# Performance work log

Measured on AMD Instinct MI355X. Metric: run time of the kernel, lower is better.

Reference implementation:

```python
import jax, jax.numpy as jnp
import numpy as np

SOS = 1
H = 1024   # hidden_size
V = 32000  # vocab_size
B = 64     # batch
S = 50     # encoder (source) length
T = 25     # decode steps (target length)


def setup_inputs() -> dict:
    key = jax.random.key(0)
    ks = jax.random.split(key, 16)
    s = 1.0 / np.sqrt(H)

    def u(k, shape):
        return jax.random.uniform(k, shape, jnp.float32, -s, s)

    return {
        "encoder_outputs": jax.random.normal(ks[0], (B, S, H), jnp.float32),
        "encoder_hidden": jax.random.normal(ks[1], (1, B, H), jnp.float32),
        "target_tensor": jax.random.randint(ks[2], (B, T), 0, V),
        "emb": jax.random.normal(ks[3], (V, H), jnp.float32),       # nn.Embedding
        "Wa": u(ks[4], (H, H)), "ba": u(ks[5], (H,)),               # attention query proj
        "Ua": u(ks[6], (H, H)), "bu": u(ks[7], (H,)),               # attention key proj
        "Va": u(ks[8], (H, 1)), "bv": u(ks[9], (1,)),               # attention score vector
        "W_ih": u(ks[10], (3 * H, 2 * H)), "b_ih": u(ks[11], (3 * H,)),  # GRU input weights
        "W_hh": u(ks[12], (3 * H, H)), "b_hh": u(ks[13], (3 * H,)),     # GRU hidden weights
        "Wout": u(ks[14], (V, H)), "bout": u(ks[15], (V,)),         # output linear
    }


def reference(encoder_outputs, encoder_hidden, target_tensor, emb,
              Wa, ba, Ua, bu, Va, bv, W_ih, b_ih, W_hh, b_hh, Wout, bout):
    # Bahdanau key projection is independent of the decode step: precompute once.
    keys_proj = encoder_outputs @ Ua.T + bu        # [B, S, H]
    h0 = encoder_hidden[0]                         # [B, H]

    # Teacher forcing: input at step i is SOS then target[:, :-1]. (Dropout in eval mode = identity.)
    sos = jnp.full((B, 1), SOS, dtype=target_tensor.dtype)
    tokens = jnp.concatenate([sos, target_tensor[:, :-1]], axis=1).T  # [T, B]

    def step(h, tok):
        x_emb = emb[tok]                                         # [B, H]
        q = h @ Wa.T + ba                                        # [B, H] (query = hidden)
        scores = jnp.tanh(q[:, None, :] + keys_proj) @ Va        # [B, S, 1]
        w = jax.nn.softmax(scores[..., 0] + bv[0], axis=-1)      # [B, S]
        context = jnp.einsum('bs,bsh->bh', w, encoder_outputs)   # [B, H]
        x = jnp.concatenate([x_emb, context], axis=-1)           # [B, 2H]
        gx = x @ W_ih.T + b_ih                                   # [B, 3H]
        gh = h @ W_hh.T + b_hh                                   # [B, 3H]
        rx, zx, nx = jnp.split(gx, 3, axis=-1)                   # PyTorch gate order r,z,n
        rh, zh, nh = jnp.split(gh, 3, axis=-1)
        r = jax.nn.sigmoid(rx + rh)
        z = jax.nn.sigmoid(zx + zh)
        n = jnp.tanh(nx + r * nh)
        h_new = (1.0 - z) * n + z * h
        logits = h_new @ Wout.T + bout                           # [B, V]
        return h_new, logits

    _, logits = jax.lax.scan(step, h0, tokens)                   # [T, B, V]
    return jnp.transpose(logits, (1, 0, 2))                      # [B, T, V]
```

## Files before the change

### kernel.cpp

```cpp
#include <hip/hip_runtime.h>
#include <hip/hip_bf16.h>

#define BB_ 64
#define SS_ 50
#define TT_ 25
#define HH_ 1024
#define VV_ 32000

typedef __bf16 bf16x8 __attribute__((ext_vector_type(8)));
typedef float f32x4 __attribute__((ext_vector_type(4)));

__device__ __forceinline__ unsigned short f2b(float f) {
  unsigned u = __float_as_uint(f);
  u = (u + 0x7FFFu + ((u >> 16) & 1u)) >> 16;
  return (unsigned short)u;
}
__device__ __forceinline__ float fast_tanh(float x) {
  float e = __expf(2.f * x);
  return 1.f - 2.f / (e + 1.f);
}
__device__ __forceinline__ float fast_sigmoid(float x) {
  return 1.f / (1.f + __expf(-x));
}
__device__ __forceinline__ void gload16(const void* g, void* l) {
  __builtin_amdgcn_global_load_lds((const __attribute__((address_space(1))) void*)g,
                                   (__attribute__((address_space(3))) void*)l, 16, 0, 0);
}
__device__ __forceinline__ bf16x8 ldb8(const unsigned short* p) {
  return *(const bf16x8*)p;
}

__global__ __launch_bounds__(256) void cvt_bf16(const float* __restrict__ src,
                                                unsigned short* __restrict__ dst, long n) {
  long i = ((long)blockIdx.x * 256 + threadIdx.x) * 4;
  if (i >= n) return;
  float4 v = *(const float4*)(src + i);
  *(ushort4*)(dst + i) = make_ushort4(f2b(v.x), f2b(v.y), f2b(v.z), f2b(v.w));
}

__global__ __launch_bounds__(256) void embed_gather(const int* __restrict__ tgt,
                                                    const float* __restrict__ emb,
                                                    unsigned short* __restrict__ X) {
  long idx = ((long)blockIdx.x * 256 + threadIdx.x) * 4;
  if (idx >= (long)1600 * HH_) return;
  int col = (int)(idx & (HH_ - 1));
  int r = (int)(idx >> 10);
  int t = r % 25;
  int tok = (t == 0) ? 1 : tgt[r - 1];
  float4 v = *(const float4*)(emb + (long)tok * HH_ + col);
  *(ushort4*)(X + idx) = make_ushort4(f2b(v.x), f2b(v.y), f2b(v.z), f2b(v.w));
}

__global__ __launch_bounds__(256) void init_h(const float* __restrict__ eh,
                                              float* __restrict__ Hf,
                                              unsigned short* __restrict__ Hb) {
  int i = (blockIdx.x * 256 + threadIdx.x) * 4;
  if (i >= BB_ * HH_) return;
  float4 v = *(const float4*)(eh + i);
  *(float4*)(Hf + i) = v;
  *(ushort4*)(Hb + i) = make_ushort4(f2b(v.x), f2b(v.y), f2b(v.z), f2b(v.w));
}

__global__ __launch_bounds__(256) void gemm128_bt(
    const unsigned short* __restrict__ A, const unsigned short* __restrict__ W,
    const float* __restrict__ bias, float* __restrict__ out, long ldo,
    int Mtiles, int ldw, int Mvalid) {
  __shared__ __align__(16) unsigned short As[128 * 32];
  __shared__ __align__(16) unsigned short Bs[128 * 32];
  int bid = blockIdx.x;
  int m0 = (bid % Mtiles) * 128;
  int n0 = (bid / Mtiles) * 128;
  int tid = threadIdx.x;
  int w = tid >> 6, l = tid & 63;
  int srow = tid >> 2, scg = tid & 3;
  int mw = (w & 1) * 64, nw = (w >> 1) * 64;

  const unsigned short* Ag0 = A + (long)(m0 + srow) * 1024 + scg * 8;
  const unsigned short* Ag1 = Ag0 + 64 * 1024;
  const unsigned short* Wg0 = W + (long)(n0 + srow) * ldw + scg * 8;
  const unsigned short* Wg1 = Wg0 + (long)64 * ldw;
  unsigned short* lA0 = As + tid * 8;
  unsigned short* lA1 = As + 2048 + tid * 8;
  unsigned short* lB0 = Bs + tid * 8;
  unsigned short* lB1 = Bs + 2048 + tid * 8;

  f32x4 zero = {0.f, 0.f, 0.f, 0.f};
  f32x4 acc[4][4];
#pragma unroll
  for (int i = 0; i < 4; ++i)
#pragma unroll
    for (int j = 0; j < 4; ++j) acc[i][j] = zero;

  for (int k0 = 0; k0 < 1024; k0 += 32) {
    __syncthreads();
    gload16(Ag0 + k0, lA0);
    gload16(Ag1 + k0, lA1);
    gload16(Wg0 + k0, lB0);
    gload16(Wg1 + k0, lB1);
    __syncthreads();
    bf16x8 af[4], bg[4];
#pragma unroll
    for (int mt = 0; mt < 4; ++mt)
      af[mt] = ldb8(As + (mw + mt * 16 + (l & 15)) * 32 + (l >> 4) * 8);
#pragma unroll
    for (int nt = 0; nt < 4; ++nt)
      bg[nt] = ldb8(Bs + (nw + nt * 16 + (l & 15)) * 32 + (l >> 4) * 8);
#pragma unroll
    for (int mt = 0; mt < 4; ++mt)
#pragma unroll
      for (int nt = 0; nt < 4; ++nt)
        acc[mt][nt] = __builtin_amdgcn_mfma_f32_16x16x32_bf16(af[mt], bg[nt], acc[mt][nt], 0, 0, 0);
  }

  int lr = (l >> 4) * 4, lc = l & 15;
#pragma unroll
  for (int nt = 0; nt < 4; ++nt) {
    int col = n0 + nw + nt * 16 + lc;
    float bv = bias[col];
#pragma unroll
    for (int mt = 0; mt < 4; ++mt) {
#pragma unroll
      for (int r = 0; r < 4; ++r) {
        int m = m0 + mw + mt * 16 + lr + r;
        if (m < Mvalid) out[(long)m * ldo + col] = acc[mt][nt][r] + bv;
      }
    }
  }
}

__global__ __launch_bounds__(256) void step_qgh(
    const unsigned short* __restrict__ Hb, const unsigned short* __restrict__ WaB,
    const unsigned short* __restrict__ WhhB, const float* __restrict__ ba,
    const float* __restrict__ bhh, float* __restrict__ Q, float* __restrict__ GH) {
  int gw = (int)((blockIdx.x * blockDim.x + threadIdx.x) >> 6);
  int l = threadIdx.x & 63;
  int m0 = (gw & 3) * 16;
  int n = (gw >> 2) * 16;
  const unsigned short* Wp;
  const float* bp;
  float* op;
  long ldo;
  if (n < 1024) { Wp = WaB + (long)n * 1024; bp = ba + n; op = Q + n; ldo = 1024; }
  else { int n2 = n - 1024; Wp = WhhB + (long)n2 * 1024; bp = bhh + n2; op = GH + n2; ldo = 3072; }
  const unsigned short* Ap = Hb + (long)(m0 + (l & 15)) * 1024 + (l >> 4) * 8;
  const unsigned short* Bp = Wp + (long)(l & 15) * 1024 + (l >> 4) * 8;
  f32x4 acc = {0.f, 0.f, 0.f, 0.f};
#pragma unroll 4
  for (int k = 0; k < 1024; k += 32)
    acc = __builtin_amdgcn_mfma_f32_16x16x32_bf16(ldb8(Ap + k), ldb8(Bp + k), acc, 0, 0, 0);
  int lc = l & 15, lr = (l >> 4) * 4;
  float bv = bp[lc];
#pragma unroll
  for (int r = 0; r < 4; ++r) op[(long)(m0 + lr + r) * ldo + lc] = acc[r] + bv;
}

__global__ __launch_bounds__(512) void step_attn(
    const float* __restrict__ Q, const float* __restrict__ KEYS,
    const float* __restrict__ Va, const float* __restrict__ enc,
    float* __restrict__ CTX, unsigned short* __restrict__ Cb) {
  int b = blockIdx.x;
  int tid = threadIdx.x, w = tid >> 6, l = tid & 63;
  __shared__ float sc[64];
  __shared__ float wgt[64];
  const float* q = Q + (long)b * HH_;
  const float* kbase = KEYS + (long)b * SS_ * HH_;
  for (int s = w; s < SS_; s += 8) {
    const float* kr = kbase + (long)s * HH_;
    float p = 0.f;
#pragma unroll
    for (int j = 0; j < 16; ++j) {
      int hh = l + j * 64;
      p += fast_tanh(q[hh] + kr[hh]) * Va[hh];
    }
#pragma unroll
    for (int off = 32; off; off >>= 1) p += __shfl_down(p, off);
    if (l == 0) sc[s] = p;
  }
  __syncthreads();
  if (tid < 64) {
    float v = (tid < SS_) ? sc[tid] : -1e30f;
    float m = v;
#pragma unroll
    for (int off = 32; off; off >>= 1) m = fmaxf(m, __shfl_down(m, off));
    m = __shfl(m, 0);
    float e = (tid < SS_) ? __expf(v - m) : 0.f;
    float ssum = e;
#pragma unroll
    for (int off = 32; off; off >>= 1) ssum += __shfl_down(ssum, off);
    ssum = __shfl(ssum, 0);
    if (tid < SS_) wgt[tid] = e / ssum;
  }
  __syncthreads();
  for (int c = tid; c < HH_; c += 512) {
    float a0 = 0.f;
    const float* ep = enc + (long)b * SS_ * HH_ + c;
#pragma unroll 10
    for (int s = 0; s < SS_; ++s) a0 += wgt[s] * ep[(long)s * HH_];
    CTX[(long)b * HH_ + c] = a0;
    Cb[(long)b * HH_ + c] = f2b(a0);
  }
}

__global__ __launch_bounds__(256) void step_gru(
    const unsigned short* __restrict__ Cb, const unsigned short* __restrict__ WihB,
    const float* __restrict__ GA, const float* __restrict__ GH,
    float* __restrict__ Hf, unsigned short* __restrict__ Hb,
    unsigned short* __restrict__ HALL, int t) {
  int gw = (int)((blockIdx.x * blockDim.x + threadIdx.x) >> 6);
  int l = threadIdx.x & 63;
  int m0 = (gw & 3) * 16;
  int n0 = (gw >> 2) * 16;
  const unsigned short* Ap = Cb + (long)(m0 + (l & 15)) * 1024 + (l >> 4) * 8;
  const unsigned short* B0 = WihB + (long)(n0 + (l & 15)) * 2048 + 1024 + (l >> 4) * 8;
  const unsigned short* B1 = B0 + (long)1024 * 2048;
  const unsigned short* B2 = B0 + (long)2048 * 2048;
  f32x4 ar = {0.f, 0.f, 0.f, 0.f}, az = ar, an = ar;
#pragma unroll 4
  for (int k = 0; k < 1024; k += 32) {
    bf16x8 a = ldb8(Ap + k);
    ar = __builtin_amdgcn_mfma_f32_16x16x32_bf16(a, ldb8(B0 + k), ar, 0, 0, 0);
    az = __builtin_amdgcn_mfma_f32_16x16x32_bf16(a, ldb8(B1 + k), az, 0, 0, 0);
    an = __builtin_amdgcn_mfma_f32_16x16x32_bf16(a, ldb8(B2 + k), an, 0, 0, 0);
  }
  int lc = l & 15, lr = (l >> 4) * 4;
  int i = n0 + lc;
#pragma unroll
  for (int r = 0; r < 4; ++r) {
    int bb = m0 + lr + r;
    long rowBT = (long)bb * 25 + t;
    const float* ga = GA + rowBT * 3072;
    const float* gh = GH + (long)bb * 3072;
    float rr = fast_sigmoid(ga[i] + ar[r] + gh[i]);
    float zz = fast_sigmoid(ga[1024 + i] + az[r] + gh[1024 + i]);
    float nn = fast_tanh(ga[2048 + i] + an[r] + rr * gh[2048 + i]);
    float hold = Hf[(long)bb * 1024 + i];
    float hnew = (1.f - zz) * nn + zz * hold;
    Hf[(long)bb * 1024 + i] = hnew;
    unsigned short hb = f2b(hnew);
    Hb[(long)bb * 1024 + i] = hb;
    HALL[rowBT * 1024 + i] = hb;
  }
}

extern "C" void kernel_launch(void* const* d_in, const int* in_sizes, int n_in,
                              void* d_out, int out_size, void* d_ws, size_t ws_size,
                              hipStream_t stream) {
  (void)in_sizes; (void)n_in; (void)out_size; (void)ws_size;
  const float* enc  = (const float*)d_in[0];
  const float* ehid = (const float*)d_in[1];
  const int*   tgt  = (const int*)d_in[2];
  const float* emb  = (const float*)d_in[3];
  const float* Wa   = (const float*)d_in[4];
  const float* ba   = (const float*)d_in[5];
  const float* Ua   = (const float*)d_in[6];
  const float* bu   = (const float*)d_in[7];
  const float* Va   = (const float*)d_in[8];
  const float* Wih  = (const float*)d_in[10];
  const float* bih  = (const float*)d_in[11];
  const float* Whh  = (const float*)d_in[12];
  const float* bhh  = (const float*)d_in[13];
  const float* Wout = (const float*)d_in[14];
  const float* bout = (const float*)d_in[15];
  float* out = (float*)d_out;

  char* p = (char*)d_ws;
  auto alloc = [&](size_t bytes) { char* r = p; p += (bytes + 255) & ~(size_t)255; return r; };
  unsigned short* WOUTB = (unsigned short*)alloc((size_t)VV_ * HH_ * 2);
  unsigned short* WIHB  = (unsigned short*)alloc((size_t)3072 * 2048 * 2);
  unsigned short* WHHB  = (unsigned short*)alloc((size_t)3072 * 1024 * 2);
  unsigned short* WAB   = (unsigned short*)alloc((size_t)1024 * 1024 * 2);
  unsigned short* UAB   = (unsigned short*)alloc((size_t)1024 * 1024 * 2);
  unsigned short* ENCB  = (unsigned short*)alloc((size_t)BB_ * SS_ * HH_ * 2);
  unsigned short* XEMB  = (unsigned short*)alloc((size_t)1664 * HH_ * 2);
  unsigned short* HALLB = (unsigned short*)alloc((size_t)1664 * HH_ * 2);
  float* KEYS = (float*)alloc((size_t)BB_ * SS_ * HH_ * 4);
  float* GA   = (float*)alloc((size_t)1600 * 3072 * 4);
  float* GHf  = (float*)alloc((size_t)BB_ * 3072 * 4);
  float* Qf   = (float*)alloc((size_t)BB_ * HH_ * 4);
  float* Hf   = (float*)alloc((size_t)BB_ * HH_ * 4);
  unsigned short* Hb = (unsigned short*)alloc((size_t)BB_ * HH_ * 2);
  float* CTX  = (float*)alloc((size_t)BB_ * HH_ * 4);
  unsigned short* CTXB = (unsigned short*)alloc((size_t)BB_ * HH_ * 2);

  auto cvt = [&](const float* s, unsigned short* d, long n) {
    cvt_bf16<<<dim3((unsigned)((n / 4 + 255) / 256)), dim3(256), 0, stream>>>(s, d, n);
  };
  cvt(Wout, WOUTB, (long)VV_ * HH_);
  cvt(Wih, WIHB, (long)3072 * 2048);
  cvt(Whh, WHHB, (long)3072 * 1024);
  cvt(Wa, WAB, (long)1024 * 1024);
  cvt(Ua, UAB, (long)1024 * 1024);
  cvt(enc, ENCB, (long)BB_ * SS_ * HH_);
  embed_gather<<<dim3(1600 * HH_ / 4 / 256), dim3(256), 0, stream>>>(tgt, emb, XEMB);
  init_h<<<dim3(BB_ * HH_ / 4 / 256), dim3(256), 0, stream>>>(ehid, Hf, Hb);

  gemm128_bt<<<dim3(25 * 8), dim3(256), 0, stream>>>(ENCB, UAB, bu, KEYS, (long)1024, 25, 1024, 3200);
  gemm128_bt<<<dim3(13 * 24), dim3(256), 0, stream>>>(XEMB, WIHB, bih, GA, (long)3072, 13, 2048, 1600);

  for (int t = 0; t < TT_; ++t) {
    step_qgh<<<dim3(256), dim3(256), 0, stream>>>(Hb, WAB, WHHB, ba, bhh, Qf, GHf);
    step_attn<<<dim3(64), dim3(512), 0, stream>>>(Qf, KEYS, Va, enc, CTX, CTXB);
    step_gru<<<dim3(64), dim3(256), 0, stream>>>(CTXB, WIHB, GA, GHf, Hf, Hb, HALLB, t);
  }

  gemm128_bt<<<dim3(13 * 250), dim3(256), 0, stream>>>(HALLB, WOUTB, bout, out, (long)VV_, 13, 1024, 1600);
}
```

Baseline: 1.817 ms.

## Fuse per-step decode kernels into one persistent cooperative kernel with grid syncs

Replaces the 75 per-step kernel launches (qgh, attention, GRU) with a single cooperative persistent kernel that loops over the decode steps and separates phases with grid.sync(). It also remaps gemm128_bt block IDs so consecutive tiles land on the same XCD, for better L2 locality. The aim is to remove launch overhead and inter-kernel gaps. In exchange, attention now runs on only 64 of the 256 blocks with 4 waves each, and the GRU phase uses only one wave per block while the others sit idle at the barriers.

```diff
diff --git a/kernel.cpp b/kernel.cpp
--- a/kernel.cpp
+++ b/kernel.cpp
@@ -1,5 +1,8 @@
 #include <hip/hip_runtime.h>
 #include <hip/hip_bf16.h>
+#include <hip/hip_cooperative_groups.h>
+
+namespace cg = cooperative_groups;
 
 #define BB_ 64
 #define SS_ 50
@@ -67,9 +70,13 @@
     int Mtiles, int ldw, int Mvalid) {
   __shared__ __align__(16) unsigned short As[128 * 32];
   __shared__ __align__(16) unsigned short Bs[128 * 32];
-  int bid = blockIdx.x;
-  int m0 = (bid % Mtiles) * 128;
-  int n0 = (bid / Mtiles) * 128;
+  int nwg = gridDim.x;
+  int orig = blockIdx.x;
+  int xcd = orig & 7, lid = orig >> 3;
+  int qq = nwg >> 3, rr = nwg & 7;
+  int wgid = (xcd < rr ? xcd * (qq + 1) : rr * (qq + 1) + (xcd - rr) * qq) + lid;
+  int m0 = (wgid % Mtiles) * 128;
+  int n0 = (wgid / Mtiles) * 128;
   int tid = threadIdx.x;
   int w = tid >> 6, l = tid & 63;
   int srow = tid >> 2, scg = tid & 3;
@@ -128,117 +135,129 @@
   }
 }
 
-__global__ __launch_bounds__(256) void step_qgh(
-    const unsigned short* __restrict__ Hb, const unsigned short* __restrict__ WaB,
-    const unsigned short* __restrict__ WhhB, const float* __restrict__ ba,
-    const float* __restrict__ bhh, float* __restrict__ Q, float* __restrict__ GH) {
-  int gw = (int)((blockIdx.x * blockDim.x + threadIdx.x) >> 6);
-  int l = threadIdx.x & 63;
-  int m0 = (gw & 3) * 16;
-  int n = (gw >> 2) * 16;
-  const unsigned short* Wp;
-  const float* bp;
-  float* op;
-  long ldo;
-  if (n < 1024) { Wp = WaB + (long)n * 1024; bp = ba + n; op = Q + n; ldo = 1024; }
-  else { int n2 = n - 1024; Wp = WhhB + (long)n2 * 1024; bp = bhh + n2; op = GH + n2; ldo = 3072; }
-  const unsigned short* Ap = Hb + (long)(m0 + (l & 15)) * 1024 + (l >> 4) * 8;
-  const unsigned short* Bp = Wp + (long)(l & 15) * 1024 + (l >> 4) * 8;
-  f32x4 acc = {0.f, 0.f, 0.f, 0.f};
-#pragma unroll 4
-  for (int k = 0; k < 1024; k += 32)
-    acc = __builtin_amdgcn_mfma_f32_16x16x32_bf16(ldb8(Ap + k), ldb8(Bp + k), acc, 0, 0, 0);
-  int lc = l & 15, lr = (l >> 4) * 4;
-  float bv = bp[lc];
-#pragma unroll
-  for (int r = 0; r < 4; ++r) op[(long)(m0 + lr + r) * ldo + lc] = acc[r] + bv;
-}
-
-__global__ __launch_bounds__(512) void step_attn(
-    const float* __restrict__ Q, const float* __restrict__ KEYS,
-    const float* __restrict__ Va, const float* __restrict__ enc,
-    float* __restrict__ CTX, unsigned short* __restrict__ Cb) {
-  int b = blockIdx.x;
-  int tid = threadIdx.x, w = tid >> 6, l = tid & 63;
+__global__ __launch_bounds__(256) void decode_loop(
+    const unsigned short* __restrict__ WaB, const unsigned short* __restrict__ WhhB,
+    const unsigned short* __restrict__ WihB, const float* __restrict__ ba,
+    const float* __restrict__ bhh, const float* __restrict__ Va,
+    const float* __restrict__ KEYS, const float* __restrict__ enc,
+    const float* __restrict__ GA, float* __restrict__ Qf, float* __restrict__ GHf,
+    unsigned short* __restrict__ CTXB, float* __restrict__ Hf,
+    unsigned short* __restrict__ Hb, unsigned short* __restrict__ HALLB) {
+  cg::grid_group grid = cg::this_grid();
   __shared__ float sc[64];
   __shared__ float wgt[64];
-  const float* q = Q + (long)b * HH_;
-  const float* kbase = KEYS + (long)b * SS_ * HH_;
-  for (int s = w; s < SS_; s += 8) {
-    const float* kr = kbase + (long)s * HH_;
-    float p = 0.f;
-#pragma unroll
-    for (int j = 0; j < 16; ++j) {
-      int hh = l + j * 64;
-      p += fast_tanh(q[hh] + kr[hh]) * Va[hh];
+
+  const int tid = threadIdx.x;
+  const int bid = blockIdx.x;
+  const int l = tid & 63;
+  const int lc = l & 15, lr4 = (l >> 4) * 4, ko = (l >> 4) * 8;
+
+  const int gw = bid * 4 + (tid >> 6);
+  const int m0 = (gw & 3) * 16;
+  const int n = (gw >> 2) * 16;
+  const unsigned short* ApH = Hb + (long)(m0 + lc) * HH_ + ko;
+  const unsigned short* B1f;
+  float* out1p;
+  long ldo1;
+  float bv1;
+  if (n < 1024) {
+    B1f = WaB + (long)(n + lc) * 1024 + ko;
+    out1p = Qf + n; ldo1 = 1024; bv1 = ba[n + lc];
+  } else {
+    B1f = WhhB + (long)(n - 1024 + lc) * 1024 + ko;
+    out1p = GHf + (n - 1024); ldo1 = 3072; bv1 = bhh[n - 1024 + lc];
+  }
+
+  const int m3 = (bid & 3) * 16;
+  const int n3 = (bid >> 2) * 16;
+  const unsigned short* Ap3 = CTXB + (long)(m3 + lc) * 1024 + ko;
+  const unsigned short* Bg0 = WihB + (long)(n3 + lc) * 2048 + 1024 + ko;
+  const unsigned short* Bg1 = Bg0 + (long)1024 * 2048;
+  const unsigned short* Bg2 = Bg0 + (long)2048 * 2048;
+  const int ig = n3 + lc;
+
+  const f32x4 zero = {0.f, 0.f, 0.f, 0.f};
+
+  for (int t = 0; t < TT_; ++t) {
+    {
+      f32x4 acc = zero;
+#pragma unroll 4
+      for (int k = 0; k < 1024; k += 32)
+        acc = __builtin_amdgcn_mfma_f32_16x16x32_bf16(ldb8(ApH + k), ldb8(B1f + k), acc, 0, 0, 0);
+#pragma unroll
+      for (int r = 0; r < 4; ++r)
+        out1p[(long)(m0 + lr4 + r) * ldo1 + lc] = acc[r] + bv1;
     }
-#pragma unroll
-    for (int off = 32; off; off >>= 1) p += __shfl_down(p, off);
-    if (l == 0) sc[s] = p;
-  }
-  __syncthreads();
-  if (tid < 64) {
-    float v = (tid < SS_) ? sc[tid] : -1e30f;
-    float m = v;
-#pragma unroll
-    for (int off = 32; off; off >>= 1) m = fmaxf(m, __shfl_down(m, off));
-    m = __shfl(m, 0);
-    float e = (tid < SS_) ? __expf(v - m) : 0.f;
-    float ssum = e;
-#pragma unroll
-    for (int off = 32; off; off >>= 1) ssum += __shfl_down(ssum, off);
-    ssum = __shfl(ssum, 0);
-    if (tid < SS_) wgt[tid] = e / ssum;
-  }
-  __syncthreads();
-  for (int c = tid; c < HH_; c += 512) {
-    float a0 = 0.f;
-    const float* ep = enc + (long)b * SS_ * HH_ + c;
+    grid.sync();
+
+    if (bid < BB_) {
+      const int b = bid, w = tid >> 6;
+      const float* q = Qf + (long)b * HH_;
+      const float* kbase = KEYS + (long)b * SS_ * HH_;
+      for (int s = w; s < SS_; s += 4) {
+        const float* kr = kbase + (long)s * HH_;
+        float p = 0.f;
+#pragma unroll
+        for (int j = 0; j < 16; ++j) {
+          int hh = l + j * 64;
+          p += fast_tanh(q[hh] + kr[hh]) * Va[hh];
+        }
+#pragma unroll
+        for (int off = 32; off; off >>= 1) p += __shfl_down(p, off);
+        if (l == 0) sc[s] = p;
+      }
+      __syncthreads();
+      if (tid < 64) {
+        float v = (tid < SS_) ? sc[tid] : -1e30f;
+        float m = v;
+#pragma unroll
+        for (int off = 32; off; off >>= 1) m = fmaxf(m, __shfl_down(m, off));
+        m = __shfl(m, 0);
+        float e = (tid < SS_) ? __expf(v - m) : 0.f;
+        float ssum = e;
+#pragma unroll
+        for (int off = 32; off; off >>= 1) ssum += __shfl_down(ssum, off);
+        ssum = __shfl(ssum, 0);
+        if (tid < SS_) wgt[tid] = e / ssum;
+      }
+      __syncthreads();
+      for (int c = tid; c < HH_; c += 256) {
+        float a0 = 0.f;
+        const float* ep = enc + (long)b * SS_ * HH_ + c;
 #pragma unroll 10
-    for (int s = 0; s < SS_; ++s) a0 += wgt[s] * ep[(long)s * HH_];
-    CTX[(long)b * HH_ + c] = a0;
-    Cb[(long)b * HH_ + c] = f2b(a0);
-  }
-}
-
-__global__ __launch_bounds__(256) void step_gru(
-    const unsigned short* __restrict__ Cb, const unsigned short* __restrict__ WihB,
-    const float* __restrict__ GA, const float* __restrict__ GH,
-    float* __restrict__ Hf, unsigned short* __restrict__ Hb,
-    unsigned short* __restrict__ HALL, int t) {
-  int gw = (int)((blockIdx.x * blockDim.x + threadIdx.x) >> 6);
-  int l = threadIdx.x & 63;
-  int m0 = (gw & 3) * 16;
-  int n0 = (gw >> 2) * 16;
-  const unsigned short* Ap = Cb + (long)(m0 + (l & 15)) * 1024 + (l >> 4) * 8;
-  const unsigned short* B0 = WihB + (long)(n0 + (l & 15)) * 2048 + 1024 + (l >> 4) * 8;
-  const unsigned short* B1 = B0 + (long)1024 * 2048;
-  const unsigned short* B2 = B0 + (long)2048 * 2048;
-  f32x4 ar = {0.f, 0.f, 0.f, 0.f}, az = ar, an = ar;
+        for (int s = 0; s < SS_; ++s) a0 += wgt[s] * ep[(long)s * HH_];
+        CTXB[(long)b * HH_ + c] = f2b(a0);
+      }
+    }
+    grid.sync();
+
+    if (tid < 64) {
+      f32x4 ar = zero, az = zero, an_ = zero;
 #pragma unroll 4
-  for (int k = 0; k < 1024; k += 32) {
-    bf16x8 a = ldb8(Ap + k);
-    ar = __builtin_amdgcn_mfma_f32_16x16x32_bf16(a, ldb8(B0 + k), ar, 0, 0, 0);
-    az = __builtin_amdgcn_mfma_f32_16x16x32_bf16(a, ldb8(B1 + k), az, 0, 0, 0);
-    an = __builtin_amdgcn_mfma_f32_16x16x32_bf16(a, ldb8(B2 + k), an, 0, 0, 0);
-  }
-  int lc = l & 15, lr = (l >> 4) * 4;
-  int i = n0 + lc;
-#pragma unroll
-  for (int r = 0; r < 4; ++r) {
-    int bb = m0 + lr + r;
-    long rowBT = (long)bb * 25 + t;
-    const float* ga = GA + rowBT * 3072;
-    const float* gh = GH + (long)bb * 3072;
-    float rr = fast_sigmoid(ga[i] + ar[r] + gh[i]);
-    float zz = fast_sigmoid(ga[1024 + i] + az[r] + gh[1024 + i]);
-    float nn = fast_tanh(ga[2048 + i] + an[r] + rr * gh[2048 + i]);
-    float hold = Hf[(long)bb * 1024 + i];
-    float hnew = (1.f - zz) * nn + zz * hold;
-    Hf[(long)bb * 1024 + i] = hnew;
-    unsigned short hb = f2b(hnew);
-    Hb[(long)bb * 1024 + i] = hb;
-    HALL[rowBT * 1024 + i] = hb;
+      for (int k = 0; k < 1024; k += 32) {
+        bf16x8 a = ldb8(Ap3 + k);
+        ar = __builtin_amdgcn_mfma_f32_16x16x32_bf16(a, ldb8(Bg0 + k), ar, 0, 0, 0);
+        az = __builtin_amdgcn_mfma_f32_16x16x32_bf16(a, ldb8(Bg1 + k), az, 0, 0, 0);
+        an_ = __builtin_amdgcn_mfma_f32_16x16x32_bf16(a, ldb8(Bg2 + k), an_, 0, 0, 0);
+      }
+#pragma unroll
+      for (int r = 0; r < 4; ++r) {
+        int bb = m3 + lr4 + r;
+        long rowBT = (long)bb * TT_ + t;
+        const float* ga = GA + rowBT * 3072;
+        const float* gh = GHf + (long)bb * 3072;
+        float rr = fast_sigmoid(ga[ig] + ar[r] + gh[ig]);
+        float zz = fast_sigmoid(ga[1024 + ig] + az[r] + gh[1024 + ig]);
+        float nn = fast_tanh(ga[2048 + ig] + an_[r] + rr * gh[2048 + ig]);
+        float hold = Hf[(long)bb * HH_ + ig];
+        float hnew = (1.f - zz) * nn + zz * hold;
+        Hf[(long)bb * HH_ + ig] = hnew;
+        unsigned short hb = f2b(hnew);
+        Hb[(long)bb * HH_ + ig] = hb;
+        HALLB[rowBT * HH_ + ig] = hb;
+      }
+    }
+    if (t < TT_ - 1) grid.sync();
   }
 }
 
@@ -279,7 +298,6 @@
   float* Qf   = (float*)alloc((size_t)BB_ * HH_ * 4);
   float* Hf   = (float*)alloc((size_t)BB_ * HH_ * 4);
   unsigned short* Hb = (unsigned short*)alloc((size_t)BB_ * HH_ * 2);
-  float* CTX  = (float*)alloc((size_t)BB_ * HH_ * 4);
   unsigned short* CTXB = (unsigned short*)alloc((size_t)BB_ * HH_ * 2);
 
   auto cvt = [&](const float* s, unsigned short* d, long n) {
@@ -297,11 +315,11 @@
   gemm128_bt<<<dim3(25 * 8), dim3(256), 0, stream>>>(ENCB, UAB, bu, KEYS, (long)1024, 25, 1024, 3200);
   gemm128_bt<<<dim3(13 * 24), dim3(256), 0, stream>>>(XEMB, WIHB, bih, GA, (long)3072, 13, 2048, 1600);
 
-  for (int t = 0; t < TT_; ++t) {
-    step_qgh<<<dim3(256), dim3(256), 0, stream>>>(Hb, WAB, WHHB, ba, bhh, Qf, GHf);
-    step_attn<<<dim3(64), dim3(512), 0, stream>>>(Qf, KEYS, Va, enc, CTX, CTXB);
-    step_gru<<<dim3(64), dim3(256), 0, stream>>>(CTXB, WIHB, GA, GHf, Hf, Hb, HALLB, t);
-  }
+  void* cargs[] = {(void*)&WAB, (void*)&WHHB, (void*)&WIHB, (void*)&ba, (void*)&bhh,
+                   (void*)&Va,  (void*)&KEYS, (void*)&enc,  (void*)&GA, (void*)&Qf,
+                   (void*)&GHf, (void*)&CTXB, (void*)&Hf,   (void*)&Hb, (void*)&HALLB};
+  hipLaunchCooperativeKernel((const void*)decode_loop, dim3(256), dim3(256),
+                             (void**)cargs, 0, stream);
 
   gemm128_bt<<<dim3(13 * 250), dim3(256), 0, stream>>>(HALLB, WOUTB, bout, out, (long)VV_, 13, 1024, 1600);
 }
```

New measurement: 5.190 ms. 2.86x slower.
